# Kernel tuning notes

Hardware: AMD Instinct MI355X
Metric: run time of the kernel (lower is better)

Reference implementation:

```python
import jax, jax.numpy as jnp
import numpy as np

N, F, T, D = 10000, 16, 12, 16
C = 1.0
MIN_NORM = 1e-15
PROJ_EPS = 4e-3  # float32 boundary eps in PoincareBall.proj


def _norm(x):
    return jnp.clip(jnp.linalg.norm(x, axis=-1, keepdims=True), MIN_NORM, None)


def artanh(x):
    return jnp.arctanh(jnp.clip(x, -1 + 1e-7, 1 - 1e-7))


def proj(x, c):
    n = _norm(x)
    maxnorm = (1.0 - PROJ_EPS) / jnp.sqrt(c)
    return jnp.where(n > maxnorm, x / n * maxnorm, x)


def expmap0(u, c):
    sc = jnp.sqrt(c)
    un = _norm(u)
    return jnp.tanh(sc * un) * u / (sc * un)


def logmap0(p, c):
    sc = jnp.sqrt(c)
    pn = _norm(p)
    return artanh(sc * pn) * p / (sc * pn)


def mobius_add(x, y, c):
    x2 = jnp.sum(x * x, -1, keepdims=True)
    y2 = jnp.sum(y * y, -1, keepdims=True)
    xy = jnp.sum(x * y, -1, keepdims=True)
    num = (1 + 2 * c * xy + c * y2) * x + (1 - c * x2) * y
    den = 1 + 2 * c * xy + c * c * x2 * y2
    return num / jnp.clip(den, MIN_NORM, None)


def mobius_matvec(m, x, c):
    sc = jnp.sqrt(c)
    xn = _norm(x)
    mx = x @ m.T
    mxn = _norm(mx)
    res = jnp.tanh(mxn / xn * artanh(sc * xn)) * mx / (mxn * sc)
    return jnp.where(jnp.all(mx == 0, axis=-1, keepdims=True), 0.0, res)


def temporal_attention(x, U1, U2, U3, be, Ve):
    # x: (B, N, F, T)
    lhs = jnp.einsum('bnft,n,fm->btm', x, U1, U2)   # (B, T, N)
    rhs = jnp.einsum('f,bnft->bnt', U3, x)          # (B, N, T)
    product = jnp.einsum('btn,bns->bts', lhs, rhs)  # (B, T, T)
    E = jnp.einsum('ij,bjs->bis', Ve, jax.nn.sigmoid(product + be))
    return jax.nn.softmax(E, axis=1)


def time_conv(x, w, b):
    # x: (B, F, N, T), kernel (1,3), padding (0,1), stride 1
    y = jax.lax.conv_general_dilated(x, w, (1, 1), ((0, 0), (1, 1)),
                                     dimension_numbers=('NCHW', 'OIHW', 'NCHW'))
    return y + b[None, :, None, None]


def hgc_layer(x_hyp, adj, w, b, c):
    # HypLinear (dropout=0 / eval mode)
    mv = proj(mobius_matvec(w, x_hyp, c), c)
    hyp_b = proj(expmap0(b.reshape(1, -1), c), c)
    res = proj(mobius_add(mv, hyp_b, c), c)
    # HypAgg (use_att=False): aggregate in tangent space at origin
    xt = logmap0(res, c)
    sup = jnp.einsum('mn,tnd->tmd', adj, xt)  # adj @ x_tangent per timestep
    agg = proj(expmap0(sup, c), c)
    # HypAct: relu, c_in == c_out (proj_tan0 is identity)
    return proj(expmap0(jax.nn.relu(logmap0(agg, c)), c), c)


def _forward(x, adj, U1a, U2a, U3a, be_a, Ve_a, U1b, U2b, U3b, be_b, Ve_b,
             conv1_w, conv1_b, conv2_w, conv2_b, hgc_w, hgc_b):
    xb = x[None]  # (1, N, F, T)
    # ---- first temporal attention + conv + hyperbolic GCN over timesteps ----
    tA = temporal_attention(xb, U1a, U2a, U3a, be_a, Ve_a)  # (1, T, T)
    x_tat = (xb.reshape(1, N * F, T) @ tA).reshape(1, N, F, T)
    x_tat = time_conv(jnp.transpose(x_tat, (0, 2, 1, 3)), conv1_w, conv1_b)  # (1, F, N, T)
    y_all = jnp.transpose(x_tat[0], (2, 1, 0))  # (T, N, F): per-timestep node features
    x_hyp = proj(expmap0(y_all, C), C)          # proj_tan0 is identity on PoincareBall
    out = hgc_layer(x_hyp, adj, hgc_w, hgc_b, C)  # (T, N, D)
    h = jnp.transpose(out, (1, 2, 0))[None]       # (1, N, D, T)
    # ---- second temporal attention + conv (this is what encode() returns) ----
    tA2 = temporal_attention(xb, U1b, U2b, U3b, be_b, Ve_b)
    x_tat2 = (xb.reshape(1, N * F, T) @ tA2).reshape(1, N, F, T)
    x_tat2 = time_conv(jnp.transpose(x_tat2, (0, 2, 1, 3)), conv2_w, conv2_b)
    final_output = jnp.transpose(x_tat2, (0, 3, 2, 1))  # (1, T, N, F)
    return final_output, h


def setup_inputs():
    key = jax.random.key(0)
    ks = jax.random.split(key, 16)

    def nrm(k, shape, scale=0.1):
        return jax.random.normal(k, shape, jnp.float32) * scale

    adj = jax.random.uniform(ks[1], (N, N), jnp.float32)
    adj = adj / jnp.sum(adj, axis=1, keepdims=True)  # row-normalized dense adjacency
    return {
        'x': jax.random.normal(ks[0], (N, F, T), jnp.float32),
        'adj': adj,
        'U1a': nrm(ks[2], (N,), 0.01), 'U2a': nrm(ks[3], (F, N), 0.01),
        'U3a': nrm(ks[4], (F,)), 'be_a': nrm(ks[5], (1, T, T)), 'Ve_a': nrm(ks[6], (T, T)),
        'U1b': nrm(ks[7], (N,), 0.01), 'U2b': nrm(ks[8], (F, N), 0.01),
        'U3b': nrm(ks[9], (F,)), 'be_b': nrm(ks[10], (1, T, T)), 'Ve_b': nrm(ks[11], (T, T)),
        'conv1_w': nrm(ks[12], (F, F, 1, 3)), 'conv1_b': jnp.zeros((F,), jnp.float32),
        'conv2_w': nrm(ks[13], (F, F, 1, 3)), 'conv2_b': jnp.zeros((F,), jnp.float32),
        'hgc_w': nrm(ks[14], (D, F)), 'hgc_b': nrm(ks[15], (D,), 0.01),
    }


def reference(x, adj, U1a, U2a, U3a, be_a, Ve_a, U1b, U2b, U3b, be_b, Ve_b,
              conv1_w, conv1_b, conv2_w, conv2_b, hgc_w, hgc_b):
    return _forward(x, adj, U1a, U2a, U3a, be_a, Ve_a, U1b, U2b, U3b, be_b, Ve_b,
                    conv1_w, conv1_b, conv2_w, conv2_b, hgc_w, hgc_b)
```

## Files before the change

### kernel.cpp

```cpp
#include <hip/hip_runtime.h>
#include <hip/hip_bf16.h>
#include <math.h>

#define NN 10000

typedef __attribute__((ext_vector_type(4))) float f32x4;
typedef __attribute__((ext_vector_type(8))) short short8v;

__device__ __forceinline__ short f2bf(float f) {
  union { float f; unsigned u; } v; v.f = f;
  unsigned u = v.u + 0x7FFFu + ((v.u >> 16) & 1u);
  return (short)(u >> 16);
}
__device__ __forceinline__ float bf2f(unsigned short h) {
  union { unsigned u; float f; } v; v.u = ((unsigned)h) << 16;
  return v.f;
}
__device__ __forceinline__ float artanh_(float xx) {
  xx = fminf(fmaxf(xx, -1.f + 1e-7f), 1.f - 1e-7f);
  return atanhf(xx);
}
__device__ __forceinline__ void proj16(float* v) {
  float s = 0.f;
#pragma unroll
  for (int i = 0; i < 16; ++i) s += v[i] * v[i];
  float n = fmaxf(sqrtf(s), 1e-15f);
  const float mxn = 1.0f - 4e-3f;
  if (n > mxn) {
    float sc = mxn / n;
#pragma unroll
    for (int i = 0; i < 16; ++i) v[i] *= sc;
  }
}
__device__ __forceinline__ short8v cvt8(const float4& u, const float4& w) {
  union { __hip_bfloat162 h; unsigned u32; } c0, c1, c2, c3;
  c0.h = __float22bfloat162_rn(make_float2(u.x, u.y));
  c1.h = __float22bfloat162_rn(make_float2(u.z, u.w));
  c2.h = __float22bfloat162_rn(make_float2(w.x, w.y));
  c3.h = __float22bfloat162_rn(make_float2(w.z, w.w));
  union { unsigned v[4]; short8v s; } r;
  r.v[0] = c0.u32; r.v[1] = c1.u32; r.v[2] = c2.u32; r.v[3] = c3.u32;
  return r.s;
}

__global__ __launch_bounds__(192) void k_attn1(
    const float* __restrict__ x,
    const float* __restrict__ U1a, const float* __restrict__ U3a,
    const float* __restrict__ U1b, const float* __restrict__ U3b,
    float* __restrict__ rhsA, float* __restrict__ rhsB,
    float* __restrict__ partAa, float* __restrict__ partAb,
    unsigned short* __restrict__ PB) {
  __shared__ float xs[16 * 193];
  int tid = threadIdx.x;
  int f_ = tid / 12, t_ = tid - f_ * 12;
  int s_ = tid >> 4, nl_ = tid & 15;
  if (blockIdx.x == 79) {
    for (int i = tid; i < 3072; i += 192) {
      int tt = i >> 8, q = i & 255;
      PB[(size_t)(312 * 12 + tt) * 512 + 256 + q] = 0;
    }
  }
  float paa = 0.f, pab = 0.f;
  for (int tb = blockIdx.x; tb < 625; tb += 80) {
    int n0 = tb * 16;
    for (int i = tid; i < 16 * 192; i += 192) {
      int a = i / 192, j = i - a * 192;
      xs[a * 193 + j] = x[(size_t)(n0 + a) * 192 + j];
    }
    __syncthreads();
    float ra = 0.f, rb = 0.f;
#pragma unroll
    for (int f = 0; f < 16; ++f) {
      float xv = xs[nl_ * 193 + f * 12 + s_];
      ra += xv * U3a[f];
      rb += xv * U3b[f];
    }
    rhsA[s_ * NN + n0 + nl_] = ra;
    rhsB[s_ * NN + n0 + nl_] = rb;
#pragma unroll
    for (int nl = 0; nl < 16; ++nl) {
      float xv = xs[nl * 193 + f_ * 12 + t_];
      paa += xv * U1a[n0 + nl];
      pab += xv * U1b[n0 + nl];
    }
    __syncthreads();
  }
  partAa[blockIdx.x * 192 + tid] = paa;
  partAb[blockIdx.x * 192 + tid] = pab;
}

__global__ __launch_bounds__(192) void k_attn2(
    const float* __restrict__ U2a, const float* __restrict__ U2b,
    const float* __restrict__ rhsA, const float* __restrict__ rhsB,
    float* __restrict__ partMa, float* __restrict__ partMb) {
  int tid = threadIdx.x;
  int f = tid / 12, s = tid - f * 12;
  int nA = blockIdx.x * 250, nE = nA + 250;
  float ma = 0.f, mb = 0.f;
  for (int n = nA; n < nE; ++n) {
    ma += U2a[f * NN + n] * rhsA[s * NN + n];
    mb += U2b[f * NN + n] * rhsB[s * NN + n];
  }
  partMa[blockIdx.x * 192 + tid] = ma;
  partMb[blockIdx.x * 192 + tid] = mb;
}

__global__ __launch_bounds__(192) void k_attn3(
    const float* __restrict__ partAa, const float* __restrict__ partAb,
    const float* __restrict__ partMa, const float* __restrict__ partMb,
    const float* __restrict__ beA, const float* __restrict__ VeA,
    const float* __restrict__ beB, const float* __restrict__ VeB,
    float* __restrict__ tAa, float* __restrict__ tAb) {
  __shared__ float aa[192], ab[192], Ma[192], Mb[192];
  __shared__ float spA[144], spB[144], EA[144], EB[144];
  int tid = threadIdx.x;
  float s1 = 0.f, s2 = 0.f, s3 = 0.f, s4 = 0.f;
  for (int b = 0; b < 80; ++b) { s1 += partAa[b * 192 + tid]; s2 += partAb[b * 192 + tid]; }
  for (int b = 0; b < 40; ++b) { s3 += partMa[b * 192 + tid]; s4 += partMb[b * 192 + tid]; }
  aa[tid] = s1; ab[tid] = s2; Ma[tid] = s3; Mb[tid] = s4;
  __syncthreads();
  if (tid < 144) {
    int j = tid / 12, s = tid - j * 12;
    float pa = 0.f, pb = 0.f;
#pragma unroll
    for (int f = 0; f < 16; ++f) {
      pa += aa[f * 12 + j] * Ma[f * 12 + s];
      pb += ab[f * 12 + j] * Mb[f * 12 + s];
    }
    spA[tid] = 1.f / (1.f + expf(-(pa + beA[tid])));
    spB[tid] = 1.f / (1.f + expf(-(pb + beB[tid])));
  }
  __syncthreads();
  if (tid < 144) {
    int i = tid / 12, s = tid - i * 12;
    float ea = 0.f, eb = 0.f;
#pragma unroll
    for (int j = 0; j < 12; ++j) {
      ea += VeA[i * 12 + j] * spA[j * 12 + s];
      eb += VeB[i * 12 + j] * spB[j * 12 + s];
    }
    EA[tid] = ea; EB[tid] = eb;
  }
  __syncthreads();
  if (tid < 144) {
    int s = tid % 12;
    float ma = -1e30f, mb = -1e30f;
#pragma unroll
    for (int k = 0; k < 12; ++k) { ma = fmaxf(ma, EA[k * 12 + s]); mb = fmaxf(mb, EB[k * 12 + s]); }
    float da = 0.f, db = 0.f;
#pragma unroll
    for (int k = 0; k < 12; ++k) { da += expf(EA[k * 12 + s] - ma); db += expf(EB[k * 12 + s] - mb); }
    tAa[tid] = expf(EA[tid] - ma) / da;
    tAb[tid] = expf(EB[tid] - mb) / db;
  }
}

__global__ __launch_bounds__(192) void k_node(
    const float* __restrict__ x,
    const float* __restrict__ tAa_g, const float* __restrict__ tAb_g,
    const float* __restrict__ w1g, const float* __restrict__ b1g,
    const float* __restrict__ w2g, const float* __restrict__ b2g,
    const float* __restrict__ hwg, const float* __restrict__ hbg,
    float* __restrict__ outF, unsigned short* __restrict__ PB) {
  __shared__ float xs[16 * 193], tbuf[16 * 193];
  __shared__ float tAa[144], tAb[144], w1[768], w2[768];
  __shared__ float cb1[16], cb2[16], hw[256], hbr[16];
  int tid = threadIdx.x;
  int nl = tid & 15, tt = tid >> 4;
  int n0 = blockIdx.x * 16;
  for (int i = tid; i < 144; i += 192) { tAa[i] = tAa_g[i]; tAb[i] = tAb_g[i]; }
  for (int i = tid; i < 768; i += 192) { w1[i] = w1g[i]; w2[i] = w2g[i]; }
  for (int i = tid; i < 256; i += 192) hw[i] = hwg[i];
  if (tid < 16) { cb1[tid] = b1g[tid]; cb2[tid] = b2g[tid]; hbr[tid] = hbg[tid]; }
  for (int i = tid; i < 16 * 192; i += 192) {
    int a = i / 192, j = i - a * 192;
    xs[a * 193 + j] = x[(size_t)(n0 + a) * 192 + j];
  }
  __syncthreads();

  float z[16];
#pragma unroll
  for (int f = 0; f < 16; ++f) {
    float v = 0.f;
#pragma unroll
    for (int s = 0; s < 12; ++s) v += xs[nl * 193 + f * 12 + s] * tAb[s * 12 + tt];
    tbuf[nl * 193 + f * 12 + tt] = v;
  }
  __syncthreads();
#pragma unroll
  for (int o = 0; o < 16; ++o) z[o] = cb2[o];
#pragma unroll
  for (int k = 0; k < 3; ++k) {
    int t2 = tt + k - 1;
    if (t2 >= 0 && t2 < 12) {
#pragma unroll
      for (int i = 0; i < 16; ++i) {
        float xv = tbuf[nl * 193 + i * 12 + t2];
#pragma unroll
        for (int o = 0; o < 16; ++o) z[o] += xv * w2[o * 48 + i * 3 + k];
      }
    }
  }
  {
    float* op = outF + (size_t)tt * (NN * 16) + (size_t)(n0 + nl) * 16;
#pragma unroll
    for (int o = 0; o < 16; ++o) op[o] = z[o];
  }
  __syncthreads();

#pragma unroll
  for (int f = 0; f < 16; ++f) {
    float v = 0.f;
#pragma unroll
    for (int s = 0; s < 12; ++s) v += xs[nl * 193 + f * 12 + s] * tAa[s * 12 + tt];
    tbuf[nl * 193 + f * 12 + tt] = v;
  }
  __syncthreads();
#pragma unroll
  for (int o = 0; o < 16; ++o) z[o] = cb1[o];
#pragma unroll
  for (int k = 0; k < 3; ++k) {
    int t2 = tt + k - 1;
    if (t2 >= 0 && t2 < 12) {
#pragma unroll
      for (int i = 0; i < 16; ++i) {
        float xv = tbuf[nl * 193 + i * 12 + t2];
#pragma unroll
        for (int o = 0; o < 16; ++o) z[o] += xv * w1[o * 48 + i * 3 + k];
      }
    }
  }
  float nz = 0.f;
#pragma unroll
  for (int i = 0; i < 16; ++i) nz += z[i] * z[i];
  nz = fmaxf(sqrtf(nz), 1e-15f);
  float sc0 = tanhf(nz) / nz;
#pragma unroll
  for (int i = 0; i < 16; ++i) z[i] *= sc0;
  proj16(z);
  float xn = 0.f;
#pragma unroll
  for (int i = 0; i < 16; ++i) xn += z[i] * z[i];
  xn = fmaxf(sqrtf(xn), 1e-15f);
  float mx[16];
#pragma unroll
  for (int d = 0; d < 16; ++d) {
    float v = 0.f;
#pragma unroll
    for (int f = 0; f < 16; ++f) v += z[f] * hw[d * 16 + f];
    mx[d] = v;
  }
  float mxr = 0.f;
#pragma unroll
  for (int d = 0; d < 16; ++d) mxr += mx[d] * mx[d];
  mxr = sqrtf(mxr);
  float mxn = fmaxf(mxr, 1e-15f);
  float rs = tanhf(mxn / xn * artanh_(xn)) / mxn;
  if (mxr == 0.f) rs = 0.f;
#pragma unroll
  for (int d = 0; d < 16; ++d) mx[d] *= rs;
  proj16(mx);
  float hb[16];
  float bn = 0.f;
#pragma unroll
  for (int i = 0; i < 16; ++i) { hb[i] = hbr[i]; bn += hb[i] * hb[i]; }
  bn = fmaxf(sqrtf(bn), 1e-15f);
  float sb = tanhf(bn) / bn;
#pragma unroll
  for (int i = 0; i < 16; ++i) hb[i] *= sb;
  proj16(hb);
  float x2 = 0.f, y2 = 0.f, xy = 0.f;
#pragma unroll
  for (int i = 0; i < 16; ++i) { x2 += mx[i] * mx[i]; y2 += hb[i] * hb[i]; xy += mx[i] * hb[i]; }
  float ca = 1.f + 2.f * xy + y2;
  float cbv = 1.f - x2;
  float den = fmaxf(1.f + 2.f * xy + x2 * y2, 1e-15f);
#pragma unroll
  for (int i = 0; i < 16; ++i) mx[i] = (ca * mx[i] + cbv * hb[i]) / den;
  proj16(mx);
  float pn = 0.f;
#pragma unroll
  for (int i = 0; i < 16; ++i) pn += mx[i] * mx[i];
  pn = fmaxf(sqrtf(pn), 1e-15f);
  float sl = artanh_(pn) / pn;
  {
    int nn2 = n0 + nl;
    int s = nn2 >> 5, c = nn2 & 31;
    unsigned short* pp = PB + (size_t)(s * 12 + tt) * 512 + (c >> 3) * 128 + (c & 7);
#pragma unroll
    for (int d = 0; d < 16; ++d)
      pp[d * 8] = (unsigned short)f2bf(mx[d] * sl);
  }
}

__global__ __launch_bounds__(256, 2) void k_gemm(
    const float* __restrict__ adj, const unsigned short* __restrict__ PB,
    unsigned short* __restrict__ partC, int S) {
  __shared__ float sA[2][128 * 32];
  __shared__ unsigned short sB[2][12 * 512];
  int bc = blockIdx.x / 79;
  int rt = blockIdx.x - bc * 79;
  int t0 = bc * S, t1 = min(313, t0 + S);
  int tid = threadIdx.x;
  int lane = tid & 63, w = tid >> 6;
  int r0 = lane & 15, kq = lane >> 4;
  int R0 = rt * 128 + w * 32;

  int arow[4], aoffF[4];
#pragma unroll
  for (int c = 0; c < 4; ++c) {
    int li = c * 256 + tid;
    int row = li >> 3;
    int off = (li & 7) * 16;
    int xa = ((row & 3) << 5) | ((row & 4) << 2);
    arow[c] = min(rt * 128 + row, NN - 1);
    aoffF[c] = (off ^ xa) >> 2;
  }

  f32x4 acc0[12], acc1[12];
  f32x4 zz = {0.f, 0.f, 0.f, 0.f};
#pragma unroll
  for (int j = 0; j < 12; ++j) { acc0[j] = zz; acc1[j] = zz; }

  auto STAGE = [&](int p, int t) {
    const unsigned short* gb = PB + (size_t)t * 6144;
#pragma unroll
    for (int c = 0; c < 3; ++c) {
      int li = c * 256 + tid;
      __builtin_amdgcn_global_load_lds((const void*)(gb + li * 8),
                                       (void*)(&sB[p][li * 8]), 16, 0, 0);
    }
#pragma unroll
    for (int c = 0; c < 4; ++c) {
      int li = c * 256 + tid;
      int fo = t * 32 + aoffF[c];
      if (fo >= NN) fo = 0;
      __builtin_amdgcn_global_load_lds((const void*)(adj + (size_t)arow[c] * NN + fo),
                                       (void*)(&sA[p][li * 4]), 16, 0, 0);
    }
  };

  int xr = ((r0 & 3) << 5) | ((r0 & 4) << 2);
  auto MM = [&](int p) {
    const char* Ab = (const char*)(sA[p]);
    float4 a00 = *(const float4*)(Ab + r0 * 128 + ((kq * 32 + 0) ^ xr));
    float4 a01 = *(const float4*)(Ab + r0 * 128 + ((kq * 32 + 16) ^ xr));
    float4 a10 = *(const float4*)(Ab + (r0 + 16) * 128 + ((kq * 32 + 0) ^ xr));
    float4 a11 = *(const float4*)(Ab + (r0 + 16) * 128 + ((kq * 32 + 16) ^ xr));
    short8v fa0 = cvt8(a00, a01);
    short8v fa1 = cvt8(a10, a11);
    const unsigned short* Bb = sB[p];
#pragma unroll
    for (int j = 0; j < 12; ++j) {
      short8v b = *((const short8v*)(Bb + j * 512) + lane);
      acc0[j] = __builtin_amdgcn_mfma_f32_16x16x32_bf16(fa0, b, acc0[j], 0, 0, 0);
      acc1[j] = __builtin_amdgcn_mfma_f32_16x16x32_bf16(fa1, b, acc1[j], 0, 0, 0);
    }
  };

  if (t0 < t1) {
    STAGE(0, t0);
    __syncthreads();
    int p = 0;
    for (int t = t0; t < t1; ++t) {
      if (t + 1 < t1) STAGE(p ^ 1, t + 1);
      MM(p);
      __syncthreads();
      p ^= 1;
    }
  }
  size_t cbase = (size_t)bc * ((size_t)NN * 192);
  int drow = kq * 4;
#pragma unroll
  for (int j = 0; j < 12; ++j) {
#pragma unroll
    for (int r = 0; r < 4; ++r) {
      int rw0 = R0 + drow + r;
      int rw1 = R0 + 16 + drow + r;
      if (rw0 < NN)
        partC[cbase + (size_t)rw0 * 192 + j * 16 + r0] = (unsigned short)f2bf(acc0[j][r]);
      if (rw1 < NN)
        partC[cbase + (size_t)rw1 * 192 + j * 16 + r0] = (unsigned short)f2bf(acc1[j][r]);
    }
  }
}

__global__ __launch_bounds__(256) void k_epi(const unsigned short* __restrict__ partC,
                                             float* __restrict__ outH, int NC) {
  int gid = blockIdx.x * 256 + threadIdx.x;
  if (gid >= NN * 12) return;
  int n = gid / 12, t = gid - n * 12;
  float sup[16];
#pragma unroll
  for (int d = 0; d < 16; ++d) sup[d] = 0.f;
  for (int c = 0; c < NC; ++c) {
    const short8v* p8 = (const short8v*)(partC + (size_t)c * (NN * 192) + (size_t)n * 192 + t * 16);
    short8v lo = p8[0], hi = p8[1];
#pragma unroll
    for (int d = 0; d < 8; ++d) sup[d] += bf2f((unsigned short)lo[d]);
#pragma unroll
    for (int d = 0; d < 8; ++d) sup[8 + d] += bf2f((unsigned short)hi[d]);
  }
  float nn_ = 0.f;
#pragma unroll
  for (int d = 0; d < 16; ++d) nn_ += sup[d] * sup[d];
  nn_ = fmaxf(sqrtf(nn_), 1e-15f);
  float s0 = tanhf(nn_) / nn_;
#pragma unroll
  for (int d = 0; d < 16; ++d) sup[d] *= s0;
  proj16(sup);
  float pn = 0.f;
#pragma unroll
  for (int d = 0; d < 16; ++d) pn += sup[d] * sup[d];
  pn = fmaxf(sqrtf(pn), 1e-15f);
  float sl = artanh_(pn) / pn;
#pragma unroll
  for (int d = 0; d < 16; ++d) sup[d] = fmaxf(sup[d] * sl, 0.f);
  float un = 0.f;
#pragma unroll
  for (int d = 0; d < 16; ++d) un += sup[d] * sup[d];
  un = fmaxf(sqrtf(un), 1e-15f);
  float se = tanhf(un) / un;
#pragma unroll
  for (int d = 0; d < 16; ++d) sup[d] *= se;
  proj16(sup);
  float* hp = outH + (size_t)n * 192 + t;
#pragma unroll
  for (int d = 0; d < 16; ++d) hp[d * 12] = sup[d];
}

extern "C" void kernel_launch(void* const* d_in, const int* in_sizes, int n_in,
                              void* d_out, int out_size, void* d_ws, size_t ws_size,
                              hipStream_t stream) {
  const float* x   = (const float*)d_in[0];
  const float* adj = (const float*)d_in[1];
  const float* U1a = (const float*)d_in[2];
  const float* U2a = (const float*)d_in[3];
  const float* U3a = (const float*)d_in[4];
  const float* bea = (const float*)d_in[5];
  const float* Vea = (const float*)d_in[6];
  const float* U1b = (const float*)d_in[7];
  const float* U2b = (const float*)d_in[8];
  const float* U3b = (const float*)d_in[9];
  const float* beb = (const float*)d_in[10];
  const float* Veb = (const float*)d_in[11];
  const float* w1  = (const float*)d_in[12];
  const float* b1  = (const float*)d_in[13];
  const float* w2  = (const float*)d_in[14];
  const float* b2  = (const float*)d_in[15];
  const float* hw  = (const float*)d_in[16];
  const float* hb  = (const float*)d_in[17];
  float* outF = (float*)d_out;
  float* outH = (float*)d_out + 1920000;

  char* ws = (char*)d_ws;
  size_t off = 0;
  auto alloc = [&](size_t bytes) {
    char* p = ws + off;
    off = (off + bytes + 255) & ~(size_t)255;
    return p;
  };
  float* rhsA   = (float*)alloc((size_t)12 * NN * 4);
  float* rhsB   = (float*)alloc((size_t)12 * NN * 4);
  float* partAa = (float*)alloc(80 * 192 * 4);
  float* partAb = (float*)alloc(80 * 192 * 4);
  float* partMa = (float*)alloc(40 * 192 * 4);
  float* partMb = (float*)alloc(40 * 192 * 4);
  float* tAa    = (float*)alloc(144 * 4);
  float* tAb    = (float*)alloc(144 * 4);
  unsigned short* PB = (unsigned short*)alloc((size_t)314 * 12 * 512 * 2);
  size_t chunkB = (size_t)NN * 192 * 2;
  size_t avail = (ws_size > off) ? (ws_size - off) : 0;
  int NC = (int)(avail / chunkB);
  if (NC > 8) NC = 8;
  if (NC < 1) NC = 1;
  unsigned short* partC = (unsigned short*)(ws + off);
  int S = (313 + NC - 1) / NC;

  k_attn1<<<80, 192, 0, stream>>>(x, U1a, U3a, U1b, U3b, rhsA, rhsB, partAa, partAb, PB);
  k_attn2<<<40, 192, 0, stream>>>(U2a, U2b, rhsA, rhsB, partMa, partMb);
  k_attn3<<<1, 192, 0, stream>>>(partAa, partAb, partMa, partMb, bea, Vea, beb, Veb, tAa, tAb);
  k_node<<<625, 192, 0, stream>>>(x, tAa, tAb, w1, b1, w2, b2, hw, hb, outF, PB);
  k_gemm<<<79 * NC, 256, 0, stream>>>(adj, PB, partC, S);
  k_epi<<<(NN * 12 + 255) / 256, 256, 0, stream>>>(partC, outH, NC);
}
```

Baseline: 263.0 us.

## Replace split-K adjacency GEMM with single-wave full-K triple-buffered kernel

The adjacency GEMM used 256-thread blocks on 128-row tiles with split-K chunks, writing bf16 partials that an epilogue summed. It now uses 313 single-wave blocks, each owning 32 rows over the full K range. Loads go through a three-stage LDS ring paced by explicit vmcnt/lgkmcnt waits, and results are written once in fp32, so the partial buffers and the epilogue reduction go away. The attention-reduction kernels also launch twice as many blocks with smaller slices. In exchange, the PB operand is re-read by four times as many row tiles, each CU runs only one wave, and 313 blocks do not split evenly across the CUs.

Result: slower. 387.0 us (+47.1%).

```diff
diff --git a/kernel.cpp b/kernel.cpp
--- a/kernel.cpp
+++ b/kernel.cpp
@@ -11,10 +11,6 @@
   union { float f; unsigned u; } v; v.f = f;
   unsigned u = v.u + 0x7FFFu + ((v.u >> 16) & 1u);
   return (short)(u >> 16);
-}
-__device__ __forceinline__ float bf2f(unsigned short h) {
-  union { unsigned u; float f; } v; v.u = ((unsigned)h) << 16;
-  return v.f;
 }
 __device__ __forceinline__ float artanh_(float xx) {
   xx = fminf(fmaxf(xx, -1.f + 1e-7f), 1.f - 1e-7f);
@@ -61,7 +57,7 @@
     }
   }
   float paa = 0.f, pab = 0.f;
-  for (int tb = blockIdx.x; tb < 625; tb += 80) {
+  for (int tb = blockIdx.x; tb < 625; tb += 160) {
     int n0 = tb * 16;
     for (int i = tid; i < 16 * 192; i += 192) {
       int a = i / 192, j = i - a * 192;
@@ -95,7 +91,7 @@
     float* __restrict__ partMa, float* __restrict__ partMb) {
   int tid = threadIdx.x;
   int f = tid / 12, s = tid - f * 12;
-  int nA = blockIdx.x * 250, nE = nA + 250;
+  int nA = blockIdx.x * 125, nE = nA + 125;
   float ma = 0.f, mb = 0.f;
   for (int n = nA; n < nE; ++n) {
     ma += U2a[f * NN + n] * rhsA[s * NN + n];
@@ -115,8 +111,8 @@
   __shared__ float spA[144], spB[144], EA[144], EB[144];
   int tid = threadIdx.x;
   float s1 = 0.f, s2 = 0.f, s3 = 0.f, s4 = 0.f;
-  for (int b = 0; b < 80; ++b) { s1 += partAa[b * 192 + tid]; s2 += partAb[b * 192 + tid]; }
-  for (int b = 0; b < 40; ++b) { s3 += partMa[b * 192 + tid]; s4 += partMb[b * 192 + tid]; }
+  for (int b = 0; b < 160; ++b) { s1 += partAa[b * 192 + tid]; s2 += partAb[b * 192 + tid]; }
+  for (int b = 0; b < 80; ++b) { s3 += partMa[b * 192 + tid]; s4 += partMb[b * 192 + tid]; }
   aa[tid] = s1; ab[tid] = s2; Ma[tid] = s3; Mb[tid] = s4;
   __syncthreads();
   if (tid < 144) {
@@ -293,28 +289,24 @@
   }
 }
 
-__global__ __launch_bounds__(256, 2) void k_gemm(
+__global__ __launch_bounds__(64) void k_gemm(
     const float* __restrict__ adj, const unsigned short* __restrict__ PB,
-    unsigned short* __restrict__ partC, int S) {
-  __shared__ float sA[2][128 * 32];
-  __shared__ unsigned short sB[2][12 * 512];
-  int bc = blockIdx.x / 79;
-  int rt = blockIdx.x - bc * 79;
-  int t0 = bc * S, t1 = min(313, t0 + S);
-  int tid = threadIdx.x;
-  int lane = tid & 63, w = tid >> 6;
+    float* __restrict__ sup) {
+  __shared__ float sA[3][32 * 32];
+  __shared__ unsigned short sB[3][12 * 512];
+  int rt = blockIdx.x;
+  int lane = threadIdx.x;
   int r0 = lane & 15, kq = lane >> 4;
-  int R0 = rt * 128 + w * 32;
-
-  int arow[4], aoffF[4];
+  int R0 = rt * 32;
+
+  int arow[4], aoff[4];
 #pragma unroll
   for (int c = 0; c < 4; ++c) {
-    int li = c * 256 + tid;
+    int li = c * 64 + lane;
     int row = li >> 3;
-    int off = (li & 7) * 16;
-    int xa = ((row & 3) << 5) | ((row & 4) << 2);
-    arow[c] = min(rt * 128 + row, NN - 1);
-    aoffF[c] = (off ^ xa) >> 2;
+    int boff = ((li & 7) * 16) ^ ((row & 7) << 4);
+    arow[c] = min(R0 + row, NN - 1);
+    aoff[c] = boff >> 2;
   }
 
   f32x4 acc0[12], acc1[12];
@@ -322,31 +314,30 @@
 #pragma unroll
   for (int j = 0; j < 12; ++j) { acc0[j] = zz; acc1[j] = zz; }
 
-  auto STAGE = [&](int p, int t) {
+  auto STAGE = [&](int t, int p) {
+#pragma unroll
+    for (int c = 0; c < 4; ++c) {
+      int fo = t * 32 + aoff[c];
+      if (fo >= NN) fo = 0;
+      __builtin_amdgcn_global_load_lds((const void*)(adj + (size_t)arow[c] * NN + fo),
+                                       (void*)(&sA[p][(c * 64 + lane) * 4]), 16, 0, 0);
+    }
     const unsigned short* gb = PB + (size_t)t * 6144;
 #pragma unroll
-    for (int c = 0; c < 3; ++c) {
-      int li = c * 256 + tid;
+    for (int c = 0; c < 12; ++c) {
+      int li = c * 64 + lane;
       __builtin_amdgcn_global_load_lds((const void*)(gb + li * 8),
                                        (void*)(&sB[p][li * 8]), 16, 0, 0);
     }
-#pragma unroll
-    for (int c = 0; c < 4; ++c) {
-      int li = c * 256 + tid;
-      int fo = t * 32 + aoffF[c];
-      if (fo >= NN) fo = 0;
-      __builtin_amdgcn_global_load_lds((const void*)(adj + (size_t)arow[c] * NN + fo),
-                                       (void*)(&sA[p][li * 4]), 16, 0, 0);
-    }
   };
 
-  int xr = ((r0 & 3) << 5) | ((r0 & 4) << 2);
+  int swz = (r0 & 7) << 4;
   auto MM = [&](int p) {
     const char* Ab = (const char*)(sA[p]);
-    float4 a00 = *(const float4*)(Ab + r0 * 128 + ((kq * 32 + 0) ^ xr));
-    float4 a01 = *(const float4*)(Ab + r0 * 128 + ((kq * 32 + 16) ^ xr));
-    float4 a10 = *(const float4*)(Ab + (r0 + 16) * 128 + ((kq * 32 + 0) ^ xr));
-    float4 a11 = *(const float4*)(Ab + (r0 + 16) * 128 + ((kq * 32 + 16) ^ xr));
+    float4 a00 = *(const float4*)(Ab + r0 * 128 + ((kq * 32 + 0) ^ swz));
+    float4 a01 = *(const float4*)(Ab + r0 * 128 + ((kq * 32 + 16) ^ swz));
+    float4 a10 = *(const float4*)(Ab + (r0 + 16) * 128 + ((kq * 32 + 0) ^ swz));
+    float4 a11 = *(const float4*)(Ab + (r0 + 16) * 128 + ((kq * 32 + 16) ^ swz));
     short8v fa0 = cvt8(a00, a01);
     short8v fa1 = cvt8(a10, a11);
     const unsigned short* Bb = sB[p];
@@ -358,18 +349,19 @@
     }
   };
 
-  if (t0 < t1) {
-    STAGE(0, t0);
-    __syncthreads();
-    int p = 0;
-    for (int t = t0; t < t1; ++t) {
-      if (t + 1 < t1) STAGE(p ^ 1, t + 1);
-      MM(p);
-      __syncthreads();
-      p ^= 1;
-    }
-  }
-  size_t cbase = (size_t)bc * ((size_t)NN * 192);
+  STAGE(0, 0); STAGE(1, 1); STAGE(2, 2);
+  int p = 0;
+  for (int t = 0; t < 310; ++t) {
+    asm volatile("s_waitcnt vmcnt(32)" ::: "memory");
+    MM(p);
+    asm volatile("s_waitcnt lgkmcnt(0)" ::: "memory");
+    STAGE(t + 3, p);
+    p = (p == 2) ? 0 : p + 1;
+  }
+  asm volatile("s_waitcnt vmcnt(32)" ::: "memory"); MM(1);
+  asm volatile("s_waitcnt vmcnt(16)" ::: "memory"); MM(2);
+  asm volatile("s_waitcnt vmcnt(0)" ::: "memory");  MM(0);
+
   int drow = kq * 4;
 #pragma unroll
   for (int j = 0; j < 12; ++j) {
@@ -377,29 +369,23 @@
     for (int r = 0; r < 4; ++r) {
       int rw0 = R0 + drow + r;
       int rw1 = R0 + 16 + drow + r;
-      if (rw0 < NN)
-        partC[cbase + (size_t)rw0 * 192 + j * 16 + r0] = (unsigned short)f2bf(acc0[j][r]);
-      if (rw1 < NN)
-        partC[cbase + (size_t)rw1 * 192 + j * 16 + r0] = (unsigned short)f2bf(acc1[j][r]);
-    }
-  }
-}
-
-__global__ __launch_bounds__(256) void k_epi(const unsigned short* __restrict__ partC,
-                                             float* __restrict__ outH, int NC) {
+      if (rw0 < NN) sup[(size_t)rw0 * 192 + j * 16 + r0] = acc0[j][r];
+      if (rw1 < NN) sup[(size_t)rw1 * 192 + j * 16 + r0] = acc1[j][r];
+    }
+  }
+}
+
+__global__ __launch_bounds__(256) void k_epi(const float* __restrict__ supg,
+                                             float* __restrict__ outH) {
   int gid = blockIdx.x * 256 + threadIdx.x;
   if (gid >= NN * 12) return;
   int n = gid / 12, t = gid - n * 12;
   float sup[16];
-#pragma unroll
-  for (int d = 0; d < 16; ++d) sup[d] = 0.f;
-  for (int c = 0; c < NC; ++c) {
-    const short8v* p8 = (const short8v*)(partC + (size_t)c * (NN * 192) + (size_t)n * 192 + t * 16);
-    short8v lo = p8[0], hi = p8[1];
-#pragma unroll
-    for (int d = 0; d < 8; ++d) sup[d] += bf2f((unsigned short)lo[d]);
-#pragma unroll
-    for (int d = 0; d < 8; ++d) sup[8 + d] += bf2f((unsigned short)hi[d]);
+  const float4* p4 = (const float4*)(supg + (size_t)n * 192 + t * 16);
+#pragma unroll
+  for (int q = 0; q < 4; ++q) {
+    float4 v = p4[q];
+    sup[q * 4 + 0] = v.x; sup[q * 4 + 1] = v.y; sup[q * 4 + 2] = v.z; sup[q * 4 + 3] = v.w;
   }
   float nn_ = 0.f;
 #pragma unroll
@@ -462,25 +448,20 @@
   };
   float* rhsA   = (float*)alloc((size_t)12 * NN * 4);
   float* rhsB   = (float*)alloc((size_t)12 * NN * 4);
-  float* partAa = (float*)alloc(80 * 192 * 4);
-  float* partAb = (float*)alloc(80 * 192 * 4);
-  float* partMa = (float*)alloc(40 * 192 * 4);
-  float* partMb = (float*)alloc(40 * 192 * 4);
+  float* partAa = (float*)alloc(160 * 192 * 4);
+  float* partAb = (float*)alloc(160 * 192 * 4);
+  float* partMa = (float*)alloc(80 * 192 * 4);
+  float* partMb = (float*)alloc(80 * 192 * 4);
   float* tAa    = (float*)alloc(144 * 4);
   float* tAb    = (float*)alloc(144 * 4);
-  unsigned short* PB = (unsigned short*)alloc((size_t)314 * 12 * 512 * 2);
-  size_t chunkB = (size_t)NN * 192 * 2;
-  size_t avail = (ws_size > off) ? (ws_size - off) : 0;
-  int NC = (int)(avail / chunkB);
-  if (NC > 8) NC = 8;
-  if (NC < 1) NC = 1;
-  unsigned short* partC = (unsigned short*)(ws + off);
-  int S = (313 + NC - 1) / NC;
-
-  k_attn1<<<80, 192, 0, stream>>>(x, U1a, U3a, U1b, U3b, rhsA, rhsB, partAa, partAb, PB);
-  k_attn2<<<40, 192, 0, stream>>>(U2a, U2b, rhsA, rhsB, partMa, partMb);
+  unsigned short* PB = (unsigned short*)alloc((size_t)313 * 12 * 512 * 2);
+  float* sup = (float*)alloc((size_t)NN * 192 * 4);
+  (void)ws_size;
+
+  k_attn1<<<160, 192, 0, stream>>>(x, U1a, U3a, U1b, U3b, rhsA, rhsB, partAa, partAb, PB);
+  k_attn2<<<80, 192, 0, stream>>>(U2a, U2b, rhsA, rhsB, partMa, partMb);
   k_attn3<<<1, 192, 0, stream>>>(partAa, partAb, partMa, partMb, bea, Vea, beb, Veb, tAa, tAb);
   k_node<<<625, 192, 0, stream>>>(x, tAa, tAb, w1, b1, w2, b2, hw, hb, outF, PB);
-  k_gemm<<<79 * NC, 256, 0, stream>>>(adj, PB, partC, S);
-  k_epi<<<(NN * 12 + 255) / 256, 256, 0, stream>>>(partC, outH, NC);
-}
+  k_gemm<<<313, 64, 0, stream>>>(adj, PB, sup);
+  k_epi<<<(NN * 12 + 255) / 256, 256, 0, stream>>>(sup, outH);
+}
```

## Replace LDS-staged GEMM with single-wave register-pipelined direct global loads

Applied to the files above, without the earlier changes.

The adjacency GEMM no longer stages A and B tiles through double-buffered shared memory in 256-thread blocks. Each 64-thread wave now owns 32 rows and loads adj and the bf16 B operand straight into registers, with a two-deep register prefetch and no block barriers. The goal is to remove LDS round-trips and __syncthreads stalls and to put more independent waves in flight to stream the large fp32 adj matrix. The cost is that every wave re-reads B from global memory and L2, and the padded PB tail now has to be zeroed in k_attn2. The attention reduction kernels also get twice as many blocks for more parallelism.

New measurement: 321.9 us. +22.4%, slower.

```diff
diff --git a/kernel.cpp b/kernel.cpp
--- a/kernel.cpp
+++ b/kernel.cpp
@@ -61,7 +61,7 @@
     }
   }
   float paa = 0.f, pab = 0.f;
-  for (int tb = blockIdx.x; tb < 625; tb += 80) {
+  for (int tb = blockIdx.x; tb < 625; tb += 160) {
     int n0 = tb * 16;
     for (int i = tid; i < 16 * 192; i += 192) {
       int a = i / 192, j = i - a * 192;
@@ -92,10 +92,15 @@
 __global__ __launch_bounds__(192) void k_attn2(
     const float* __restrict__ U2a, const float* __restrict__ U2b,
     const float* __restrict__ rhsA, const float* __restrict__ rhsB,
-    float* __restrict__ partMa, float* __restrict__ partMb) {
+    float* __restrict__ partMa, float* __restrict__ partMb,
+    unsigned short* __restrict__ PB) {
   int tid = threadIdx.x;
+  for (int i = tid; i < 960; i += 192) {
+    int idx = blockIdx.x * 960 + i;
+    if (idx < 67584) PB[1923072 + idx] = 0;
+  }
   int f = tid / 12, s = tid - f * 12;
-  int nA = blockIdx.x * 250, nE = nA + 250;
+  int nA = blockIdx.x * 125, nE = nA + 125;
   float ma = 0.f, mb = 0.f;
   for (int n = nA; n < nE; ++n) {
     ma += U2a[f * NN + n] * rhsA[s * NN + n];
@@ -115,8 +120,8 @@
   __shared__ float spA[144], spB[144], EA[144], EB[144];
   int tid = threadIdx.x;
   float s1 = 0.f, s2 = 0.f, s3 = 0.f, s4 = 0.f;
-  for (int b = 0; b < 80; ++b) { s1 += partAa[b * 192 + tid]; s2 += partAb[b * 192 + tid]; }
-  for (int b = 0; b < 40; ++b) { s3 += partMa[b * 192 + tid]; s4 += partMb[b * 192 + tid]; }
+  for (int b = 0; b < 160; ++b) { s1 += partAa[b * 192 + tid]; s2 += partAb[b * 192 + tid]; }
+  for (int b = 0; b < 80; ++b) { s3 += partMa[b * 192 + tid]; s4 += partMb[b * 192 + tid]; }
   aa[tid] = s1; ab[tid] = s2; Ma[tid] = s3; Mb[tid] = s4;
   __syncthreads();
   if (tid < 144) {
@@ -293,82 +298,62 @@
   }
 }
 
-__global__ __launch_bounds__(256, 2) void k_gemm(
+__global__ __launch_bounds__(64) void k_gemm(
     const float* __restrict__ adj, const unsigned short* __restrict__ PB,
     unsigned short* __restrict__ partC, int S) {
-  __shared__ float sA[2][128 * 32];
-  __shared__ unsigned short sB[2][12 * 512];
-  int bc = blockIdx.x / 79;
-  int rt = blockIdx.x - bc * 79;
-  int t0 = bc * S, t1 = min(313, t0 + S);
-  int tid = threadIdx.x;
-  int lane = tid & 63, w = tid >> 6;
+  int bc = blockIdx.x / 313;
+  int rt = blockIdx.x - bc * 313;
+  int g0 = bc * S, g1 = min(g0 + S, 320);
+  int lane = threadIdx.x;
   int r0 = lane & 15, kq = lane >> 4;
-  int R0 = rt * 128 + w * 32;
-
-  int arow[4], aoffF[4];
-#pragma unroll
-  for (int c = 0; c < 4; ++c) {
-    int li = c * 256 + tid;
-    int row = li >> 3;
-    int off = (li & 7) * 16;
-    int xa = ((row & 3) << 5) | ((row & 4) << 2);
-    arow[c] = min(rt * 128 + row, NN - 1);
-    aoffF[c] = (off ^ xa) >> 2;
-  }
+  int R0 = rt * 32;
+  int row0 = min(R0 + r0, NN - 1), row1 = min(R0 + 16 + r0, NN - 1);
+  const float* pa0 = adj + (size_t)row0 * NN;
+  const float* pa1 = adj + (size_t)row1 * NN;
+  int cq = kq * 8;
 
   f32x4 acc0[12], acc1[12];
   f32x4 zz = {0.f, 0.f, 0.f, 0.f};
 #pragma unroll
   for (int j = 0; j < 12; ++j) { acc0[j] = zz; acc1[j] = zz; }
 
-  auto STAGE = [&](int p, int t) {
-    const unsigned short* gb = PB + (size_t)t * 6144;
-#pragma unroll
-    for (int c = 0; c < 3; ++c) {
-      int li = c * 256 + tid;
-      __builtin_amdgcn_global_load_lds((const void*)(gb + li * 8),
-                                       (void*)(&sB[p][li * 8]), 16, 0, 0);
-    }
-#pragma unroll
-    for (int c = 0; c < 4; ++c) {
-      int li = c * 256 + tid;
-      int fo = t * 32 + aoffF[c];
-      if (fo >= NN) fo = 0;
-      __builtin_amdgcn_global_load_lds((const void*)(adj + (size_t)arow[c] * NN + fo),
-                                       (void*)(&sA[p][li * 4]), 16, 0, 0);
-    }
+  auto LA = [&](int t, float4* a) {
+    int col = t * 32 + cq;
+    if (col + 8 > NN) col = 0;
+    a[0] = *(const float4*)(pa0 + col);
+    a[1] = *(const float4*)(pa0 + col + 4);
+    a[2] = *(const float4*)(pa1 + col);
+    a[3] = *(const float4*)(pa1 + col + 4);
   };
-
-  int xr = ((r0 & 3) << 5) | ((r0 & 4) << 2);
-  auto MM = [&](int p) {
-    const char* Ab = (const char*)(sA[p]);
-    float4 a00 = *(const float4*)(Ab + r0 * 128 + ((kq * 32 + 0) ^ xr));
-    float4 a01 = *(const float4*)(Ab + r0 * 128 + ((kq * 32 + 16) ^ xr));
-    float4 a10 = *(const float4*)(Ab + (r0 + 16) * 128 + ((kq * 32 + 0) ^ xr));
-    float4 a11 = *(const float4*)(Ab + (r0 + 16) * 128 + ((kq * 32 + 16) ^ xr));
-    short8v fa0 = cvt8(a00, a01);
-    short8v fa1 = cvt8(a10, a11);
-    const unsigned short* Bb = sB[p];
+  auto LB = [&](int t, short8v* b) {
+    const short8v* g = (const short8v*)(PB + (size_t)t * 6144) + lane;
+#pragma unroll
+    for (int j = 0; j < 12; ++j) b[j] = g[j * 64];
+  };
+  auto MMX = [&](const float4* a, const short8v* b) {
+    short8v f0 = cvt8(a[0], a[1]);
+    short8v f1 = cvt8(a[2], a[3]);
 #pragma unroll
     for (int j = 0; j < 12; ++j) {
-      short8v b = *((const short8v*)(Bb + j * 512) + lane);
-      acc0[j] = __builtin_amdgcn_mfma_f32_16x16x32_bf16(fa0, b, acc0[j], 0, 0, 0);
-      acc1[j] = __builtin_amdgcn_mfma_f32_16x16x32_bf16(fa1, b, acc1[j], 0, 0, 0);
+      acc0[j] = __builtin_amdgcn_mfma_f32_16x16x32_bf16(f0, b[j], acc0[j], 0, 0, 0);
+      acc1[j] = __builtin_amdgcn_mfma_f32_16x16x32_bf16(f1, b[j], acc1[j], 0, 0, 0);
     }
   };
 
-  if (t0 < t1) {
-    STAGE(0, t0);
-    __syncthreads();
-    int p = 0;
-    for (int t = t0; t < t1; ++t) {
-      if (t + 1 < t1) STAGE(p ^ 1, t + 1);
-      MM(p);
-      __syncthreads();
-      p ^= 1;
-    }
-  }
+  float4 xa[4], ya[4];
+  short8v bb[12];
+  LB(g0, bb);
+  LA(g0, xa);
+  LA(g0 + 1, ya);
+  for (int t = g0; t < g1; t += 2) {
+    MMX(xa, bb);
+    LB(t + 1, bb);
+    LA(t + 2, xa);
+    MMX(ya, bb);
+    LB(t + 2, bb);
+    LA(t + 3, ya);
+  }
+
   size_t cbase = (size_t)bc * ((size_t)NN * 192);
   int drow = kq * 4;
 #pragma unroll
@@ -462,25 +447,25 @@
   };
   float* rhsA   = (float*)alloc((size_t)12 * NN * 4);
   float* rhsB   = (float*)alloc((size_t)12 * NN * 4);
-  float* partAa = (float*)alloc(80 * 192 * 4);
-  float* partAb = (float*)alloc(80 * 192 * 4);
-  float* partMa = (float*)alloc(40 * 192 * 4);
-  float* partMb = (float*)alloc(40 * 192 * 4);
+  float* partAa = (float*)alloc(160 * 192 * 4);
+  float* partAb = (float*)alloc(160 * 192 * 4);
+  float* partMa = (float*)alloc(80 * 192 * 4);
+  float* partMb = (float*)alloc(80 * 192 * 4);
   float* tAa    = (float*)alloc(144 * 4);
   float* tAb    = (float*)alloc(144 * 4);
-  unsigned short* PB = (unsigned short*)alloc((size_t)314 * 12 * 512 * 2);
+  unsigned short* PB = (unsigned short*)alloc((size_t)324 * 6144 * 2);
   size_t chunkB = (size_t)NN * 192 * 2;
   size_t avail = (ws_size > off) ? (ws_size - off) : 0;
   int NC = (int)(avail / chunkB);
   if (NC > 8) NC = 8;
   if (NC < 1) NC = 1;
   unsigned short* partC = (unsigned short*)(ws + off);
-  int S = (313 + NC - 1) / NC;
-
-  k_attn1<<<80, 192, 0, stream>>>(x, U1a, U3a, U1b, U3b, rhsA, rhsB, partAa, partAb, PB);
-  k_attn2<<<40, 192, 0, stream>>>(U2a, U2b, rhsA, rhsB, partMa, partMb);
+  int S = ((320 + NC - 1) / NC + 1) & ~1;
+
+  k_attn1<<<160, 192, 0, stream>>>(x, U1a, U3a, U1b, U3b, rhsA, rhsB, partAa, partAb, PB);
+  k_attn2<<<80, 192, 0, stream>>>(U2a, U2b, rhsA, rhsB, partMa, partMb, PB);
   k_attn3<<<1, 192, 0, stream>>>(partAa, partAb, partMa, partMb, bea, Vea, beb, Veb, tAa, tAb);
   k_node<<<625, 192, 0, stream>>>(x, tAa, tAb, w1, b1, w2, b2, hw, hb, outF, PB);
-  k_gemm<<<79 * NC, 256, 0, stream>>>(adj, PB, partC, S);
+  k_gemm<<<313 * NC, 64, 0, stream>>>(adj, PB, partC, S);
   k_epi<<<(NN * 12 + 255) / 256, 256, 0, stream>>>(partC, outH, NC);
 }
```

## Triple-buffer adjacency tiles in GEMM with explicit vmcnt waits; widen attention grids

Applied to the files above, without the earlier changes.

The bf16 MFMA GEMM moves to dynamic shared memory. The adjacency A tiles are now triple-buffered and prefetched two steps ahead, while the B tiles stay double-buffered one step ahead. Explicit s_waitcnt vmcnt counts and raw s_barriers replace __syncthreads, so only the current tile's loads must land before compute and more global-to-LDS traffic stays in flight. Separately, the attention reduction kernels use twice as many blocks with smaller per-block ranges, which doubles the partial sums k_attn3 has to reduce. The hand-counted waits are fragile, and the larger LDS footprint per block may limit occupancy.

Result: faster. 241.5 us (-8.2%).

```diff
diff --git a/kernel.cpp b/kernel.cpp
--- a/kernel.cpp
+++ b/kernel.cpp
@@ -61,7 +61,7 @@
     }
   }
   float paa = 0.f, pab = 0.f;
-  for (int tb = blockIdx.x; tb < 625; tb += 80) {
+  for (int tb = blockIdx.x; tb < 625; tb += 160) {
     int n0 = tb * 16;
     for (int i = tid; i < 16 * 192; i += 192) {
       int a = i / 192, j = i - a * 192;
@@ -95,7 +95,7 @@
     float* __restrict__ partMa, float* __restrict__ partMb) {
   int tid = threadIdx.x;
   int f = tid / 12, s = tid - f * 12;
-  int nA = blockIdx.x * 250, nE = nA + 250;
+  int nA = blockIdx.x * 125, nE = nA + 125;
   float ma = 0.f, mb = 0.f;
   for (int n = nA; n < nE; ++n) {
     ma += U2a[f * NN + n] * rhsA[s * NN + n];
@@ -115,8 +115,8 @@
   __shared__ float spA[144], spB[144], EA[144], EB[144];
   int tid = threadIdx.x;
   float s1 = 0.f, s2 = 0.f, s3 = 0.f, s4 = 0.f;
-  for (int b = 0; b < 80; ++b) { s1 += partAa[b * 192 + tid]; s2 += partAb[b * 192 + tid]; }
-  for (int b = 0; b < 40; ++b) { s3 += partMa[b * 192 + tid]; s4 += partMb[b * 192 + tid]; }
+  for (int b = 0; b < 160; ++b) { s1 += partAa[b * 192 + tid]; s2 += partAb[b * 192 + tid]; }
+  for (int b = 0; b < 80; ++b) { s3 += partMa[b * 192 + tid]; s4 += partMb[b * 192 + tid]; }
   aa[tid] = s1; ab[tid] = s2; Ma[tid] = s3; Mb[tid] = s4;
   __syncthreads();
   if (tid < 144) {
@@ -296,11 +296,11 @@
 __global__ __launch_bounds__(256, 2) void k_gemm(
     const float* __restrict__ adj, const unsigned short* __restrict__ PB,
     unsigned short* __restrict__ partC, int S) {
-  __shared__ float sA[2][128 * 32];
-  __shared__ unsigned short sB[2][12 * 512];
+  extern __shared__ char smem[];
   int bc = blockIdx.x / 79;
   int rt = blockIdx.x - bc * 79;
   int t0 = bc * S, t1 = min(313, t0 + S);
+  int ns = t1 - t0;
   int tid = threadIdx.x;
   int lane = tid & 63, w = tid >> 6;
   int r0 = lane & 15, kq = lane >> 4;
@@ -322,53 +322,64 @@
 #pragma unroll
   for (int j = 0; j < 12; ++j) { acc0[j] = zz; acc1[j] = zz; }
 
-  auto STAGE = [&](int p, int t) {
+  auto STAGE_B = [&](int q, int t) {
     const unsigned short* gb = PB + (size_t)t * 6144;
+    char* dst = smem + 49152 + q * 12288;
 #pragma unroll
     for (int c = 0; c < 3; ++c) {
       int li = c * 256 + tid;
       __builtin_amdgcn_global_load_lds((const void*)(gb + li * 8),
-                                       (void*)(&sB[p][li * 8]), 16, 0, 0);
-    }
+                                       (void*)(dst + li * 16), 16, 0, 0);
+    }
+  };
+  auto STAGE_A = [&](int p, int t) {
+    char* dst = smem + p * 16384;
 #pragma unroll
     for (int c = 0; c < 4; ++c) {
       int li = c * 256 + tid;
       int fo = t * 32 + aoffF[c];
       if (fo >= NN) fo = 0;
       __builtin_amdgcn_global_load_lds((const void*)(adj + (size_t)arow[c] * NN + fo),
-                                       (void*)(&sA[p][li * 4]), 16, 0, 0);
+                                       (void*)(dst + li * 16), 16, 0, 0);
     }
   };
 
   int xr = ((r0 & 3) << 5) | ((r0 & 4) << 2);
-  auto MM = [&](int p) {
-    const char* Ab = (const char*)(sA[p]);
+  auto MM = [&](int t) {
+    const char* Ab = smem + (t % 3) * 16384;
+    const char* Bb = smem + 49152 + (t & 1) * 12288;
     float4 a00 = *(const float4*)(Ab + r0 * 128 + ((kq * 32 + 0) ^ xr));
     float4 a01 = *(const float4*)(Ab + r0 * 128 + ((kq * 32 + 16) ^ xr));
     float4 a10 = *(const float4*)(Ab + (r0 + 16) * 128 + ((kq * 32 + 0) ^ xr));
     float4 a11 = *(const float4*)(Ab + (r0 + 16) * 128 + ((kq * 32 + 16) ^ xr));
     short8v fa0 = cvt8(a00, a01);
     short8v fa1 = cvt8(a10, a11);
-    const unsigned short* Bb = sB[p];
 #pragma unroll
     for (int j = 0; j < 12; ++j) {
-      short8v b = *((const short8v*)(Bb + j * 512) + lane);
+      short8v b = *(const short8v*)(Bb + j * 1024 + lane * 16);
       acc0[j] = __builtin_amdgcn_mfma_f32_16x16x32_bf16(fa0, b, acc0[j], 0, 0, 0);
       acc1[j] = __builtin_amdgcn_mfma_f32_16x16x32_bf16(fa1, b, acc1[j], 0, 0, 0);
     }
   };
 
-  if (t0 < t1) {
-    STAGE(0, t0);
-    __syncthreads();
-    int p = 0;
-    for (int t = t0; t < t1; ++t) {
-      if (t + 1 < t1) STAGE(p ^ 1, t + 1);
-      MM(p);
-      __syncthreads();
-      p ^= 1;
-    }
-  }
+  STAGE_B(0, t0);
+  STAGE_A(0, t0);
+  if (ns > 1) STAGE_A(1 % 3, t0 + 1);
+
+  for (int i = 0; i < ns; ++i) {
+    if (i + 1 < ns) STAGE_B((i + 1) & 1, t0 + i + 1);
+    if (i + 2 < ns) STAGE_A((i + 2) % 3, t0 + i + 2);
+    if (i + 2 < ns)      asm volatile("s_waitcnt vmcnt(11)" ::: "memory");
+    else if (i + 1 < ns) asm volatile("s_waitcnt vmcnt(7)" ::: "memory");
+    else                 asm volatile("s_waitcnt vmcnt(0)" ::: "memory");
+    __builtin_amdgcn_sched_barrier(0);
+    __builtin_amdgcn_s_barrier();
+    MM(i);
+    asm volatile("s_waitcnt lgkmcnt(0)" ::: "memory");
+    __builtin_amdgcn_sched_barrier(0);
+    __builtin_amdgcn_s_barrier();
+  }
+
   size_t cbase = (size_t)bc * ((size_t)NN * 192);
   int drow = kq * 4;
 #pragma unroll
@@ -462,13 +473,13 @@
   };
   float* rhsA   = (float*)alloc((size_t)12 * NN * 4);
   float* rhsB   = (float*)alloc((size_t)12 * NN * 4);
-  float* partAa = (float*)alloc(80 * 192 * 4);
-  float* partAb = (float*)alloc(80 * 192 * 4);
-  float* partMa = (float*)alloc(40 * 192 * 4);
-  float* partMb = (float*)alloc(40 * 192 * 4);
+  float* partAa = (float*)alloc(160 * 192 * 4);
+  float* partAb = (float*)alloc(160 * 192 * 4);
+  float* partMa = (float*)alloc(80 * 192 * 4);
+  float* partMb = (float*)alloc(80 * 192 * 4);
   float* tAa    = (float*)alloc(144 * 4);
   float* tAb    = (float*)alloc(144 * 4);
-  unsigned short* PB = (unsigned short*)alloc((size_t)314 * 12 * 512 * 2);
+  unsigned short* PB = (unsigned short*)alloc((size_t)314 * 6144 * 2);
   size_t chunkB = (size_t)NN * 192 * 2;
   size_t avail = (ws_size > off) ? (ws_size - off) : 0;
   int NC = (int)(avail / chunkB);
@@ -477,10 +488,13 @@
   unsigned short* partC = (unsigned short*)(ws + off);
   int S = (313 + NC - 1) / NC;
 
-  k_attn1<<<80, 192, 0, stream>>>(x, U1a, U3a, U1b, U3b, rhsA, rhsB, partAa, partAb, PB);
-  k_attn2<<<40, 192, 0, stream>>>(U2a, U2b, rhsA, rhsB, partMa, partMb);
+  (void)hipFuncSetAttribute((const void*)k_gemm,
+                            hipFuncAttributeMaxDynamicSharedMemorySize, 73728);
+
+  k_attn1<<<160, 192, 0, stream>>>(x, U1a, U3a, U1b, U3b, rhsA, rhsB, partAa, partAb, PB);
+  k_attn2<<<80, 192, 0, stream>>>(U2a, U2b, rhsA, rhsB, partMa, partMb);
   k_attn3<<<1, 192, 0, stream>>>(partAa, partAb, partMa, partMb, bea, Vea, beb, Veb, tAa, tAb);
   k_node<<<625, 192, 0, stream>>>(x, tAa, tAb, w1, b1, w2, b2, hw, hb, outF, PB);
-  k_gemm<<<79 * NC, 256, 0, stream>>>(adj, PB, partC, S);
+  k_gemm<<<79 * NC, 256, 73728, stream>>>(adj, PB, partC, S);
   k_epi<<<(NN * 12 + 255) / 256, 256, 0, stream>>>(partC, outH, NC);
 }
```
